# Performance work log

Hardware: AMD Instinct MI355X
Metric: run time of the kernel (lower is better)

## Reference

```python
import jax, jax.numpy as jnp
import numpy as np

INPUT_DIM, HIDDEN_DIM, N_CLASSES = 512, 256, 2
TOP_RATIO, MIN_PATCHES, K_INST = 0.7, 128, 8
B, N = 4, 16384


def setup_inputs() -> dict:
    key = jax.random.key(0)
    ks = jax.random.split(key, 10)
    D, H, C = INPUT_DIM, HIDDEN_DIM, N_CLASSES
    s = lambda fan: 1.0 / np.sqrt(fan)
    return {
        "features": jax.random.normal(ks[0], (B, N, D), dtype=jnp.float32),
        # attention_net: Linear(D->H) (dropout is identity in eval)
        "Wa": jax.random.uniform(ks[1], (D, H), minval=-s(D), maxval=s(D), dtype=jnp.float32),
        "ba": jax.random.uniform(ks[2], (H,), minval=-s(D), maxval=s(D), dtype=jnp.float32),
        # per-class attention branches: Linear(H->1), stacked over classes
        "Wbr": jax.random.uniform(ks[3], (C, H), minval=-s(H), maxval=s(H), dtype=jnp.float32),
        "bbr": jax.random.uniform(ks[4], (C,), minval=-s(H), maxval=s(H), dtype=jnp.float32),
        # per-class instance classifiers: Linear(D->H) -> ReLU -> Linear(H->2)
        "W1": jax.random.uniform(ks[5], (C, D, H), minval=-s(D), maxval=s(D), dtype=jnp.float32),
        "b1": jax.random.uniform(ks[6], (C, H), minval=-s(D), maxval=s(D), dtype=jnp.float32),
        "W2": jax.random.uniform(ks[7], (C, H, 2), minval=-s(H), maxval=s(H), dtype=jnp.float32),
        "b2": jax.random.uniform(ks[8], (C, 2), minval=-s(H), maxval=s(H), dtype=jnp.float32),
    }


def reference(features, Wa, ba, Wbr, bbr, W1, b1, W2, b2):
    Bb, Nn, D = features.shape
    C = Wbr.shape[0]

    # ---- compute_attention ----
    h = jax.nn.relu(features @ Wa + ba)                       # (B,N,H)
    a_logits = jnp.einsum('bnh,ch->bcn', h, Wbr) + bbr[None, :, None]
    attn_all = jax.nn.softmax(a_logits, axis=-1)              # (B,C,N)
    combined = attn_all.mean(axis=1)                          # (B,N)

    # ---- per-sample top-k selection (k static under jit) ----
    k = min(max(int(Nn * TOP_RATIO), MIN_PATCHES), Nn)
    _, sel_idx = jax.lax.top_k(combined, k)                   # (B,k)
    sel_idx = jnp.sort(sel_idx, axis=-1)
    selected = jnp.take_along_axis(features, sel_idx[..., None], axis=1)  # (B,k,D)

    # ---- instance clustering loss (vectorized over B x C) ----
    kk = min(K_INST, Nn // 2)
    _, top_idx = jax.lax.top_k(attn_all, kk)                  # (B,C,kk)
    _, bot_idx = jax.lax.top_k(-attn_all, kk)                 # largest=False
    both_idx = jnp.concatenate([top_idx, bot_idx], axis=-1)   # (B,C,2kk)
    inst = features[jnp.arange(Bb)[:, None, None], both_idx]  # (B,C,2kk,D)
    h1 = jax.nn.relu(jnp.einsum('bckd,cdh->bckh', inst, W1) + b1[None, :, None, :])
    logits = jnp.einsum('bckh,cho->bcko', h1, W2) + b2[None, :, None, :]  # (B,C,2kk,2)
    labels = jnp.concatenate([jnp.ones(kk, jnp.int32), jnp.zeros(kk, jnp.int32)])
    logp = jax.nn.log_softmax(logits, axis=-1)
    ce = -jnp.take_along_axis(
        logp, jnp.broadcast_to(labels[None, None, :, None], (Bb, C, 2 * kk, 1)), axis=-1
    )[..., 0]                                                 # (B,C,2kk)
    cl_loss = ce.mean(axis=-1).sum() / (Bb * C)

    return selected, combined, sel_idx, cl_loss
```

## Files before the change

### kernel.cpp

```cpp
#include <hip/hip_runtime.h>

#define NB 4
#define NP 16384
#define DD 512
#define HH 256
#define CC 2
#define KSEL 11468
#define TOTP (NB*NP)
#define BCAP 4096

#define OFF_COMB (NB*KSEL*DD)
#define OFF_IDX  (OFF_COMB + NB*NP)
#define OFF_LOSS (OFF_IDX + NB*KSEL)

#define WS_ALOGIT 0
#define WS_ATTN   (NB*CC*NP)
#define WS_SELIDX (2*NB*CC*NP)
#define WS_MZ     (WS_SELIDX + NB*KSEL)
#define WS_BCNT   (WS_MZ + 16)
#define WS_BLIST  (WS_BCNT + 4)
#define WS_TOP16  (WS_BLIST + NB*BCAP)
#define WS_CE     (WS_TOP16 + 128)

typedef __attribute__((ext_vector_type(8))) short short8x;
typedef __attribute__((ext_vector_type(4))) float f32x4;

__device__ __forceinline__ unsigned short f2bf(float x){
  unsigned u = __float_as_uint(x);
  unsigned r = (u + 0x7FFFu + ((u >> 16) & 1u)) >> 16;
  return (unsigned short)r;
}

__global__ __launch_bounds__(256) void waconv_kernel(
    const float* __restrict__ Wa, unsigned short* __restrict__ WaT)
{
  __shared__ float tile[32][33];
  const int tx = threadIdx.x, ty = threadIdx.y;
  const int k0 = blockIdx.x * 32, n0 = blockIdx.y * 32;
  #pragma unroll
  for (int i=0;i<4;++i)
    tile[ty+8*i][tx] = Wa[(size_t)(k0+ty+8*i)*HH + n0 + tx];
  __syncthreads();
  #pragma unroll
  for (int i=0;i<4;++i)
    WaT[(size_t)(n0+ty+8*i)*DD + k0 + tx] = f2bf(tile[tx][ty+8*i]);
}

__global__ __launch_bounds__(512) void gemm_mfma_kernel(
    const float* __restrict__ feat, const unsigned short* __restrict__ WaT,
    const float* __restrict__ ba, const float* __restrict__ Wbr,
    const float* __restrict__ bbr, float* __restrict__ aL)
{
  __shared__ __attribute__((aligned(16))) unsigned char smem[65536];
  __shared__ float sBA[HH], sW0[HH], sW1[HH];
  unsigned char* sA = smem;
  unsigned char* sB = smem + 16384;

  const int tid  = threadIdx.x;
  const int lane = tid & 63;
  const int wid  = tid >> 6;
  const int wm = wid >> 2, wn = wid & 3;
  const int fr = lane & 15, fq = lane >> 4;
  const int p0 = blockIdx.x * 128;
  const float bb0 = bbr[0], bb1 = bbr[1];

  if (tid < HH){ sBA[tid] = ba[tid]; sW0[tid] = Wbr[tid]; sW1[tid] = Wbr[HH+tid]; }

  f32x4 acc[4][4];
  #pragma unroll
  for (int i=0;i<4;++i)
    #pragma unroll
    for (int j=0;j<4;++j)
      acc[i][j] = (f32x4){0.f,0.f,0.f,0.f};

  const int am = tid >> 2, akq = (tid & 3) * 16;
  const int bn = tid >> 1, bhf = tid & 1;

  for (int k0 = 0; k0 < DD; k0 += 64){
    __syncthreads();
    {
      const float4* src = reinterpret_cast<const float4*>(
          feat + (size_t)(p0 + am)*DD + k0 + akq);
      float4 v0 = src[0], v1 = src[1], v2 = src[2], v3 = src[3];
      unsigned short u[16];
      u[0]=f2bf(v0.x); u[1]=f2bf(v0.y); u[2]=f2bf(v0.z); u[3]=f2bf(v0.w);
      u[4]=f2bf(v1.x); u[5]=f2bf(v1.y); u[6]=f2bf(v1.z); u[7]=f2bf(v1.w);
      u[8]=f2bf(v2.x); u[9]=f2bf(v2.y); u[10]=f2bf(v2.z); u[11]=f2bf(v2.w);
      u[12]=f2bf(v3.x); u[13]=f2bf(v3.y); u[14]=f2bf(v3.z); u[15]=f2bf(v3.w);
      uint4 w0, w1;
      w0.x = (unsigned)u[0] | ((unsigned)u[1]<<16);
      w0.y = (unsigned)u[2] | ((unsigned)u[3]<<16);
      w0.z = (unsigned)u[4] | ((unsigned)u[5]<<16);
      w0.w = (unsigned)u[6] | ((unsigned)u[7]<<16);
      w1.x = (unsigned)u[8] | ((unsigned)u[9]<<16);
      w1.y = (unsigned)u[10] | ((unsigned)u[11]<<16);
      w1.z = (unsigned)u[12] | ((unsigned)u[13]<<16);
      w1.w = (unsigned)u[14] | ((unsigned)u[15]<<16);
      const int swz = (am & 7) << 4;
      *reinterpret_cast<uint4*>(sA + (((am*128) + akq*2) ^ swz)) = w0;
      *reinterpret_cast<uint4*>(sA + (((am*128) + akq*2 + 16) ^ swz)) = w1;
    }
    {
      const uint4* src = reinterpret_cast<const uint4*>(
          WaT + (size_t)bn*DD + k0 + bhf*32);
      uint4 q0 = src[0], q1 = src[1], q2 = src[2], q3 = src[3];
      const int swz = (bn & 7) << 4;
      const int base = bn*128 + bhf*64;
      *reinterpret_cast<uint4*>(sB + ((base     ) ^ swz)) = q0;
      *reinterpret_cast<uint4*>(sB + ((base + 16) ^ swz)) = q1;
      *reinterpret_cast<uint4*>(sB + ((base + 32) ^ swz)) = q2;
      *reinterpret_cast<uint4*>(sB + ((base + 48) ^ swz)) = q3;
    }
    __syncthreads();
    #pragma unroll
    for (int kf = 0; kf < 2; ++kf){
      short8x af[4], bf[4];
      #pragma unroll
      for (int mf = 0; mf < 4; ++mf){
        int m_loc = wm*64 + mf*16 + fr;
        int off = ((m_loc*128 + kf*64 + fq*16) ^ ((m_loc & 7) << 4));
        af[mf] = *reinterpret_cast<const short8x*>(sA + off);
      }
      #pragma unroll
      for (int nf = 0; nf < 4; ++nf){
        int n_loc = wn*64 + nf*16 + fr;
        int off = ((n_loc*128 + kf*64 + fq*16) ^ ((n_loc & 7) << 4));
        bf[nf] = *reinterpret_cast<const short8x*>(sB + off);
      }
      #pragma unroll
      for (int mf = 0; mf < 4; ++mf)
        #pragma unroll
        for (int nf = 0; nf < 4; ++nf)
          acc[mf][nf] = __builtin_amdgcn_mfma_f32_16x16x32_bf16(
              af[mf], bf[nf], acc[mf][nf], 0, 0, 0);
    }
  }
  __syncthreads();

  float* hS = reinterpret_cast<float*>(smem);
  #pragma unroll
  for (int mh = 0; mh < 2; ++mh){
    if (wm == mh){
      #pragma unroll
      for (int mf = 0; mf < 4; ++mf)
        #pragma unroll
        for (int nf = 0; nf < 4; ++nf)
          #pragma unroll
          for (int r = 0; r < 4; ++r){
            int row = mf*16 + fq*4 + r;
            int col = wn*64 + nf*16 + fr;
            hS[row*256 + col] = acc[mf][nf][r];
          }
    }
    __syncthreads();
    {
      const int row = tid >> 3, cg = tid & 7;
      float s0 = 0.f, s1 = 0.f;
      #pragma unroll
      for (int j = 0; j < 8; ++j){
        int col = cg*4 + j*32;
        float4 hv = *reinterpret_cast<const float4*>(&hS[row*256 + col]);
        float xs[4] = {hv.x, hv.y, hv.z, hv.w};
        #pragma unroll
        for (int u = 0; u < 4; ++u){
          int ccol = col + u;
          float x = fmaxf(xs[u] + sBA[ccol], 0.f);
          s0 += x * sW0[ccol];
          s1 += x * sW1[ccol];
        }
      }
      s0 += __shfl_xor(s0,1); s1 += __shfl_xor(s1,1);
      s0 += __shfl_xor(s0,2); s1 += __shfl_xor(s1,2);
      s0 += __shfl_xor(s0,4); s1 += __shfl_xor(s1,4);
      if (cg == 0){
        int p = p0 + mh*64 + row;
        int b = p >> 14, nl = p & (NP-1);
        aL[((size_t)b*CC + 0)*NP + nl] = s0 + bb0;
        aL[((size_t)b*CC + 1)*NP + nl] = s1 + bb1;
      }
    }
    __syncthreads();
  }
}

__global__ __launch_bounds__(1024) void smstat_kernel(
    const float* __restrict__ aL, float* __restrict__ mz)
{
  __shared__ float  s_redf[16];
  __shared__ double s_redd[16];
  __shared__ float  s_max;
  const int tid = threadIdx.x;
  const int lane = tid & 63, wid = tid >> 6;
  const int r = blockIdx.x;
  const float* a = aL + (size_t)r*NP;
  float m = -1e30f;
  for (int n=tid; n<NP; n+=1024) m = fmaxf(m, a[n]);
  #pragma unroll
  for (int off=1; off<64; off<<=1) m = fmaxf(m, __shfl_xor(m, off));
  if (lane==0) s_redf[wid]=m;
  __syncthreads();
  if (tid==0){ float mm=s_redf[0]; for(int w=1;w<16;++w) mm=fmaxf(mm,s_redf[w]); s_max=mm; }
  __syncthreads();
  m = s_max;
  double ls = 0.0;
  for (int n=tid;n<NP;n+=1024) ls += (double)expf(a[n]-m);
  #pragma unroll
  for (int off=1; off<64; off<<=1) ls += __shfl_xor(ls, off);
  if (lane==0) s_redd[wid]=ls;
  __syncthreads();
  if (tid==0){
    double t=0; for(int w=0;w<16;++w) t+=s_redd[w];
    mz[r*2+0]=m; mz[r*2+1]=(float)(1.0/t);
  }
}

#define SKW 1028
__global__ __launch_bounds__(1024) void selTF_kernel(
    const float* __restrict__ aL, const float* __restrict__ mz,
    float* __restrict__ attn, float* __restrict__ comb,
    int* __restrict__ bcnt, int* __restrict__ blist)
{
  __shared__ unsigned s_bits[16*SKW];
  __shared__ unsigned s_red[16];
  __shared__ unsigned s_bcast;
  __shared__ int s_cnt;
  const int tid = threadIdx.x;
  const int b = blockIdx.x;
  const int lane = tid & 63, wid = tid >> 6;
  const float m0 = mz[b*4+0], iz0 = mz[b*4+1], m1 = mz[b*4+2], iz1 = mz[b*4+3];
  const float* a0 = aL + ((size_t)b*CC + 0)*NP;
  const float* a1 = aL + ((size_t)b*CC + 1)*NP;
  float* o0 = attn + ((size_t)b*CC + 0)*NP;
  float* o1 = attn + ((size_t)b*CC + 1)*NP;
  float* oc = comb + (size_t)b*NP;
  for (int j=0;j<16;++j){
    int n = tid + j*1024;
    float e0 = expf(a0[n]-m0)*iz0;
    float e1 = expf(a1[n]-m1)*iz1;
    o0[n]=e0; o1[n]=e1;
    float cv = 0.5f*(e0+e1);
    oc[n]=cv;
    s_bits[(n & 15)*SKW + (n >> 4)] = __float_as_uint(cv);
  }
  if (tid==0) s_cnt = 0;
  __syncthreads();
  unsigned cur = 0;
  for (int bit=31; bit>=12; --bit){
    unsigned trial = cur | (1u<<bit);
    int c = 0;
    #pragma unroll
    for (int j=0;j<16;++j) c += (s_bits[j*SKW + tid] >= trial) ? 1 : 0;
    #pragma unroll
    for (int off=1; off<64; off<<=1) c += __shfl_xor(c, off);
    if (lane==0) s_red[wid] = (unsigned)c;
    __syncthreads();
    if (tid==0){ unsigned t=0; for(int w=0;w<16;++w) t+=s_red[w]; s_bcast=t; }
    __syncthreads();
    if (s_bcast >= KSEL) cur = trial;
    __syncthreads();
  }
  const float Tv = __uint_as_float(cur);
  const float lo = Tv*0.989f, hi = Tv*1.0115f;
  #pragma unroll
  for (int e=0;e<16;++e){
    float v = __uint_as_float(s_bits[e*SKW + tid]);
    if (v >= lo && v <= hi){
      int s = atomicAdd(&s_cnt, 1);
      if (s < BCAP) blist[b*BCAP + s] = tid*16 + e;
    }
  }
  __syncthreads();
  if (tid==0) bcnt[b] = (s_cnt < BCAP) ? s_cnt : BCAP;
}

__global__ __launch_bounds__(256) void recomp_kernel(
    const float* __restrict__ feat, const float* __restrict__ Wa,
    const float* __restrict__ ba, const float* __restrict__ Wbr,
    const float* __restrict__ bbr, const float* __restrict__ mz,
    const int* __restrict__ bcnt, const int* __restrict__ blist,
    float* __restrict__ comb)
{
  __shared__ float fS[DD];
  __shared__ float r0[4], r1[4];
  const int tid = threadIdx.x;
  const int b = blockIdx.x >> 12;
  const int s = blockIdx.x & (BCAP-1);
  if (s >= bcnt[b]) return;
  const int lane = tid & 63, wid = tid >> 6;
  const float m0 = mz[b*4+0], iz0 = mz[b*4+1], m1 = mz[b*4+2], iz1 = mz[b*4+3];
  const int n = blist[b*BCAP + s];
  if (tid < 128){
    float4 v = *reinterpret_cast<const float4*>(feat + ((size_t)b*NP + n)*DD + tid*4);
    *reinterpret_cast<float4*>(&fS[tid*4]) = v;
  }
  __syncthreads();
  float a0=0.f,a1=0.f,a2=0.f,a3=0.f;
  #pragma unroll 4
  for (int d=0; d<DD; d+=4){
    a0 += fS[d+0]*Wa[(size_t)(d+0)*HH + tid];
    a1 += fS[d+1]*Wa[(size_t)(d+1)*HH + tid];
    a2 += fS[d+2]*Wa[(size_t)(d+2)*HH + tid];
    a3 += fS[d+3]*Wa[(size_t)(d+3)*HH + tid];
  }
  float h = fmaxf((a0+a1)+(a2+a3) + ba[tid], 0.f);
  float p0 = h*Wbr[tid], p1 = h*Wbr[HH+tid];
  #pragma unroll
  for (int off=1; off<64; off<<=1){ p0+=__shfl_xor(p0,off); p1+=__shfl_xor(p1,off); }
  if (lane==0){ r0[wid]=p0; r1[wid]=p1; }
  __syncthreads();
  if (tid==0){
    float l0 = (r0[0]+r0[1])+(r0[2]+r0[3]) + bbr[0];
    float l1 = (r1[0]+r1[1])+(r1[2]+r1[3]) + bbr[1];
    comb[(size_t)b*NP + n] = 0.5f*(expf(l0-m0)*iz0 + expf(l1-m1)*iz1);
  }
}

__global__ __launch_bounds__(1024) void select_kernel(
    const float* __restrict__ comb, float* __restrict__ outIdxF,
    int* __restrict__ selIdx)
{
  __shared__ unsigned s_bits[16*SKW];
  __shared__ unsigned s_red[16];
  __shared__ unsigned s_scan[1024];
  __shared__ unsigned s_bcast;
  const int tid = threadIdx.x;
  const int b = blockIdx.x;
  const int lane = tid & 63, wid = tid >> 6;
  const float* row = comb + (size_t)b*NP;
  for (int j=0;j<16;++j){
    int n = tid + j*1024;
    s_bits[(n & 15)*SKW + (n >> 4)] = __float_as_uint(row[n]);
  }
  __syncthreads();
  unsigned cur = 0;
  for (int bit=31; bit>=0; --bit){
    unsigned trial = cur | (1u<<bit);
    int c = 0;
    #pragma unroll
    for (int j=0;j<16;++j) c += (s_bits[j*SKW + tid] >= trial) ? 1 : 0;
    #pragma unroll
    for (int off=1; off<64; off<<=1) c += __shfl_xor(c, off);
    if (lane==0) s_red[wid] = (unsigned)c;
    __syncthreads();
    if (tid==0){ unsigned t=0; for(int w=0;w<16;++w) t+=s_red[w]; s_bcast=t; }
    __syncthreads();
    if (s_bcast >= KSEL) cur = trial;
    __syncthreads();
  }
  const unsigned T = cur;
  {
    int c = 0;
    #pragma unroll
    for (int j=0;j<16;++j) c += (s_bits[j*SKW + tid] > T) ? 1 : 0;
    #pragma unroll
    for (int off=1; off<64; off<<=1) c += __shfl_xor(c, off);
    if (lane==0) s_red[wid] = (unsigned)c;
    __syncthreads();
    if (tid==0){ unsigned t=0; for(int w=0;w<16;++w) t+=s_red[w]; s_bcast=t; }
    __syncthreads();
  }
  const int extra = KSEL - (int)s_bcast;
  __syncthreads();
  int eqc=0;
  #pragma unroll
  for (int e=0;e<16;++e) eqc += (s_bits[e*SKW + tid]==T) ? 1 : 0;
  s_scan[tid]=(unsigned)eqc;
  __syncthreads();
  for (int off=1; off<1024; off<<=1){
    unsigned v = (tid>=off)? s_scan[tid-off] : 0u;
    __syncthreads();
    s_scan[tid]+=v;
    __syncthreads();
  }
  const int eqBase = (int)s_scan[tid] - eqc;
  __syncthreads();
  int eq=eqBase, sc=0;
  #pragma unroll
  for (int e=0;e<16;++e){
    unsigned v = s_bits[e*SKW + tid];
    if (v==T){ if (eq<extra) sc++; eq++; }
    else if (v>T) sc++;
  }
  s_scan[tid]=(unsigned)sc;
  __syncthreads();
  for (int off=1; off<1024; off<<=1){
    unsigned v = (tid>=off)? s_scan[tid-off] : 0u;
    __syncthreads();
    s_scan[tid]+=v;
    __syncthreads();
  }
  int pos = (int)s_scan[tid] - sc;
  eq=eqBase;
  #pragma unroll
  for (int e=0;e<16;++e){
    unsigned v = s_bits[e*SKW + tid];
    int f=0;
    if (v==T){ if (eq<extra) f=1; eq++; }
    else if (v>T) f=1;
    if (f){
      int n = tid*16 + e;
      outIdxF[(size_t)b*KSEL + pos] = (float)n;
      selIdx[(size_t)b*KSEL + pos] = n;
      pos++;
    }
  }
}

__global__ __launch_bounds__(256) void gather_kernel(
    const float* __restrict__ feat, const int* __restrict__ selIdx,
    float* __restrict__ outSel)
{
  const int tid = threadIdx.x;
  const int row = blockIdx.x*2 + (tid>>7);
  const int c4 = tid & 127;
  const int b = row / KSEL;
  const int idx = selIdx[row];
  const float4 v = *reinterpret_cast<const float4*>(feat + ((size_t)b*NP + idx)*DD + c4*4);
  *reinterpret_cast<float4*>(outSel + (size_t)row*DD + c4*4) = v;
}

__global__ __launch_bounds__(256) void top16_kernel(
    const float* __restrict__ attn, int* __restrict__ top16)
{
  __shared__ unsigned long long wkT[4][8];
  __shared__ unsigned long long wkB[4][8];
  const int tid = threadIdx.x;
  const int bid = blockIdx.x;
  const int lane = tid & 63, wid = tid >> 6;
  const float* a = attn + (size_t)bid*NP;

  unsigned long long t8[8], b8[8];
  #pragma unroll
  for (int i=0;i<8;++i){ t8[i]=0ull; b8[i]=~0ull; }

  for (int j=0;j<16;++j){
    const int n4 = tid + 256*j;
    const float4 v = *reinterpret_cast<const float4*>(a + 4*n4);
    const float xs[4] = {v.x, v.y, v.z, v.w};
    #pragma unroll
    for (int q=0;q<4;++q){
      const int n = 4*n4 + q;
      const unsigned vb = __float_as_uint(xs[q]);
      unsigned long long kt = ((unsigned long long)vb<<32) | (unsigned)(NP-1-n);
      if (kt > t8[7]){
        t8[7]=kt;
        #pragma unroll
        for (int i=7;i>0;--i){ if (t8[i]>t8[i-1]){ unsigned long long t=t8[i-1]; t8[i-1]=t8[i]; t8[i]=t; } }
      }
      unsigned long long kb = ((unsigned long long)vb<<32) | (unsigned)n;
      if (kb < b8[7]){
        b8[7]=kb;
        #pragma unroll
        for (int i=7;i>0;--i){ if (b8[i]<b8[i-1]){ unsigned long long t=b8[i-1]; b8[i-1]=b8[i]; b8[i]=t; } }
      }
    }
  }

  #pragma unroll
  for (int pick=0; pick<8; ++pick){
    unsigned long long loc = t8[0];
    #pragma unroll
    for (int i=1;i<8;++i) loc = t8[i]>loc ? t8[i] : loc;
    #pragma unroll
    for (int off=1; off<64; off<<=1){ unsigned long long o=__shfl_xor(loc,off); loc=o>loc?o:loc; }
    if (lane==0) wkT[wid][pick]=loc;
    #pragma unroll
    for (int i=0;i<8;++i) if (t8[i]==loc) t8[i]=0ull;
  }
  #pragma unroll
  for (int pick=0; pick<8; ++pick){
    unsigned long long loc = b8[0];
    #pragma unroll
    for (int i=1;i<8;++i) loc = b8[i]<loc ? b8[i] : loc;
    #pragma unroll
    for (int off=1; off<64; off<<=1){ unsigned long long o=__shfl_xor(loc,off); loc=o<loc?o:loc; }
    if (lane==0) wkB[wid][pick]=loc;
    #pragma unroll
    for (int i=0;i<8;++i) if (b8[i]==loc) b8[i]=~0ull;
  }
  __syncthreads();

  if (wid==0){
    unsigned long long k = (lane<32) ? wkT[lane>>3][lane&7] : 0ull;
    #pragma unroll
    for (int pick=0; pick<8; ++pick){
      unsigned long long loc = k;
      #pragma unroll
      for (int off=1; off<64; off<<=1){ unsigned long long o=__shfl_xor(loc,off); loc=o>loc?o:loc; }
      if (k==loc) k=0ull;
      if (lane==0) top16[bid*16+pick] = NP-1-(int)(loc & 0xFFFFFFFFull);
    }
    unsigned long long kb = (lane<32) ? wkB[lane>>3][lane&7] : ~0ull;
    #pragma unroll
    for (int pick=0; pick<8; ++pick){
      unsigned long long loc = kb;
      #pragma unroll
      for (int off=1; off<64; off<<=1){ unsigned long long o=__shfl_xor(loc,off); loc=o<loc?o:loc; }
      if (kb==loc) kb=~0ull;
      if (lane==0) top16[bid*16+8+pick] = (int)(loc & 0xFFFFFFFFull);
    }
  }
}

__global__ __launch_bounds__(256) void mlp_kernel(
    const float* __restrict__ feat, const float* __restrict__ W1,
    const float* __restrict__ b1, const float* __restrict__ W2,
    const float* __restrict__ b2, const int* __restrict__ top16,
    float* __restrict__ cews)
{
  __shared__ float fS[DD];
  __shared__ float r0[4], r1[4];
  const int tid = threadIdx.x;
  const int bid = blockIdx.x;
  const int r = bid & 15, c = (bid >> 4) & 1, b = bid >> 5;
  const int lane = tid & 63, wid = tid >> 6;
  const int gi = top16[(b*2+c)*16 + r];
  if (tid < 128){
    float4 v = *reinterpret_cast<const float4*>(feat + ((size_t)b*NP + gi)*DD + tid*4);
    *reinterpret_cast<float4*>(&fS[tid*4]) = v;
  }
  __syncthreads();
  const float* w1c = W1 + (size_t)c*DD*HH;
  float a0=0.f,a1=0.f,a2=0.f,a3=0.f;
  #pragma unroll 4
  for (int d=0; d<DD; d+=4){
    a0 += fS[d+0]*w1c[(size_t)(d+0)*HH + tid];
    a1 += fS[d+1]*w1c[(size_t)(d+1)*HH + tid];
    a2 += fS[d+2]*w1c[(size_t)(d+2)*HH + tid];
    a3 += fS[d+3]*w1c[(size_t)(d+3)*HH + tid];
  }
  float h = fmaxf((a0+a1)+(a2+a3) + b1[c*HH+tid], 0.f);
  float p0 = h*W2[(size_t)(c*HH+tid)*2 + 0];
  float p1 = h*W2[(size_t)(c*HH+tid)*2 + 1];
  #pragma unroll
  for (int off=1; off<64; off<<=1){ p0+=__shfl_xor(p0,off); p1+=__shfl_xor(p1,off); }
  if (lane==0){ r0[wid]=p0; r1[wid]=p1; }
  __syncthreads();
  if (tid==0){
    float l0 = (r0[0]+r0[1])+(r0[2]+r0[3]) + b2[c*2+0];
    float l1 = (r1[0]+r1[1])+(r1[2]+r1[3]) + b2[c*2+1];
    float mm = fmaxf(l0,l1);
    float lse = mm + logf(expf(l0-mm)+expf(l1-mm));
    float chosen = (r<8) ? l1 : l0;
    cews[bid] = lse - chosen;
  }
}

__global__ void loss_kernel(const float* __restrict__ cews, float* __restrict__ out_loss){
  if (threadIdx.x==0 && blockIdx.x==0){
    float s=0.f;
    for (int i=0;i<128;++i) s += cews[i];
    out_loss[0] = s / 128.0f;
  }
}

extern "C" void kernel_launch(void* const* d_in, const int* in_sizes, int n_in,
                              void* d_out, int out_size, void* d_ws, size_t ws_size,
                              hipStream_t stream) {
  const float* feat = (const float*)d_in[0];
  const float* Wa   = (const float*)d_in[1];
  const float* ba   = (const float*)d_in[2];
  const float* Wbr  = (const float*)d_in[3];
  const float* bbr  = (const float*)d_in[4];
  const float* W1   = (const float*)d_in[5];
  const float* b1   = (const float*)d_in[6];
  const float* W2   = (const float*)d_in[7];
  const float* b2   = (const float*)d_in[8];
  float* out = (float*)d_out;
  float* ws  = (float*)d_ws;

  float* a_logits = ws + WS_ALOGIT;
  float* attn     = ws + WS_ATTN;
  int*   selIdx   = (int*)(ws + WS_SELIDX);
  float* mz       = ws + WS_MZ;
  int*   bcnt     = (int*)(ws + WS_BCNT);
  int*   blist    = (int*)(ws + WS_BLIST);
  int*   top16    = (int*)(ws + WS_TOP16);
  float* cews     = ws + WS_CE;

  unsigned short* WaT = (unsigned short*)d_out;

  hipLaunchKernelGGL(waconv_kernel, dim3(DD/32, HH/32), dim3(32,8), 0, stream,
                     Wa, WaT);
  hipLaunchKernelGGL(gemm_mfma_kernel, dim3(TOTP/128), dim3(512), 0, stream,
                     feat, WaT, ba, Wbr, bbr, a_logits);
  hipLaunchKernelGGL(smstat_kernel, dim3(NB*CC), dim3(1024), 0, stream,
                     a_logits, mz);
  hipLaunchKernelGGL(selTF_kernel, dim3(NB), dim3(1024), 0, stream,
                     a_logits, mz, attn, out + OFF_COMB, bcnt, blist);
  hipLaunchKernelGGL(recomp_kernel, dim3(NB*BCAP), dim3(256), 0, stream,
                     feat, Wa, ba, Wbr, bbr, mz, bcnt, blist, out + OFF_COMB);
  hipLaunchKernelGGL(select_kernel, dim3(NB), dim3(1024), 0, stream,
                     out + OFF_COMB, out + OFF_IDX, selIdx);
  hipLaunchKernelGGL(gather_kernel, dim3(NB*KSEL/2), dim3(256), 0, stream,
                     feat, selIdx, out);
  hipLaunchKernelGGL(top16_kernel, dim3(NB*CC), dim3(256), 0, stream,
                     attn, top16);
  hipLaunchKernelGGL(mlp_kernel, dim3(NB*CC*16), dim3(256), 0, stream,
                     feat, W1, b1, W2, b2, top16, cews);
  hipLaunchKernelGGL(loss_kernel, dim3(1), dim3(64), 0, stream,
                     cews, out + OFF_LOSS);
}
```

Before: 283.7 us.

## Keep top-k radix values in registers and cut block barriers per bit

The threshold-selection and index-selection kernels now keep each thread's 16 contiguous values in registers, loaded with float4, instead of staging them in a padded shared-memory array. The per-bit radix count uses a double-buffered reduction slot, so each bit needs one barrier instead of three. The 1024-entry shared-memory prefix scans are replaced by wave shuffle scans plus a per-wave sum. This removes shared-memory traffic and most synchronisation in the serial bit loops, at the cost of more register pressure and a redundant 16-way sum in every thread.

```diff
diff --git a/kernel.cpp b/kernel.cpp
--- a/kernel.cpp
+++ b/kernel.cpp
@@ -214,15 +214,12 @@
   }
 }
 
-#define SKW 1028
 __global__ __launch_bounds__(1024) void selTF_kernel(
     const float* __restrict__ aL, const float* __restrict__ mz,
     float* __restrict__ attn, float* __restrict__ comb,
     int* __restrict__ bcnt, int* __restrict__ blist)
 {
-  __shared__ unsigned s_bits[16*SKW];
-  __shared__ unsigned s_red[16];
-  __shared__ unsigned s_bcast;
+  __shared__ unsigned s_red[2][16];
   __shared__ int s_cnt;
   const int tid = threadIdx.x;
   const int b = blockIdx.x;
@@ -233,40 +230,52 @@
   float* o0 = attn + ((size_t)b*CC + 0)*NP;
   float* o1 = attn + ((size_t)b*CC + 1)*NP;
   float* oc = comb + (size_t)b*NP;
-  for (int j=0;j<16;++j){
-    int n = tid + j*1024;
-    float e0 = expf(a0[n]-m0)*iz0;
-    float e1 = expf(a1[n]-m1)*iz1;
-    o0[n]=e0; o1[n]=e1;
-    float cv = 0.5f*(e0+e1);
-    oc[n]=cv;
-    s_bits[(n & 15)*SKW + (n >> 4)] = __float_as_uint(cv);
+  const int n0 = tid*16;
+
+  unsigned v[16];
+  #pragma unroll
+  for (int g=0; g<4; ++g){
+    float4 qa = *reinterpret_cast<const float4*>(a0 + n0 + g*4);
+    float4 qb = *reinterpret_cast<const float4*>(a1 + n0 + g*4);
+    float4 E0, E1, CV;
+    E0.x = expf(qa.x-m0)*iz0; E1.x = expf(qb.x-m1)*iz1; CV.x = 0.5f*(E0.x+E1.x);
+    E0.y = expf(qa.y-m0)*iz0; E1.y = expf(qb.y-m1)*iz1; CV.y = 0.5f*(E0.y+E1.y);
+    E0.z = expf(qa.z-m0)*iz0; E1.z = expf(qb.z-m1)*iz1; CV.z = 0.5f*(E0.z+E1.z);
+    E0.w = expf(qa.w-m0)*iz0; E1.w = expf(qb.w-m1)*iz1; CV.w = 0.5f*(E0.w+E1.w);
+    *reinterpret_cast<float4*>(o0 + n0 + g*4) = E0;
+    *reinterpret_cast<float4*>(o1 + n0 + g*4) = E1;
+    *reinterpret_cast<float4*>(oc + n0 + g*4) = CV;
+    v[g*4+0]=__float_as_uint(CV.x);
+    v[g*4+1]=__float_as_uint(CV.y);
+    v[g*4+2]=__float_as_uint(CV.z);
+    v[g*4+3]=__float_as_uint(CV.w);
   }
   if (tid==0) s_cnt = 0;
-  __syncthreads();
+
   unsigned cur = 0;
+  #pragma unroll 1
   for (int bit=31; bit>=12; --bit){
     unsigned trial = cur | (1u<<bit);
     int c = 0;
     #pragma unroll
-    for (int j=0;j<16;++j) c += (s_bits[j*SKW + tid] >= trial) ? 1 : 0;
+    for (int i=0;i<16;++i) c += (v[i] >= trial) ? 1 : 0;
     #pragma unroll
     for (int off=1; off<64; off<<=1) c += __shfl_xor(c, off);
-    if (lane==0) s_red[wid] = (unsigned)c;
+    if (lane==0) s_red[bit&1][wid] = (unsigned)c;
     __syncthreads();
-    if (tid==0){ unsigned t=0; for(int w=0;w<16;++w) t+=s_red[w]; s_bcast=t; }
-    __syncthreads();
-    if (s_bcast >= KSEL) cur = trial;
-    __syncthreads();
+    unsigned tot=0;
+    #pragma unroll
+    for (int w=0;w<16;++w) tot += s_red[bit&1][w];
+    if (tot >= KSEL) cur = trial;
   }
   const float Tv = __uint_as_float(cur);
   const float lo = Tv*0.989f, hi = Tv*1.0115f;
   #pragma unroll
-  for (int e=0;e<16;++e){
-    float v = __uint_as_float(s_bits[e*SKW + tid]);
-    if (v >= lo && v <= hi){
+  for (int i=0;i<16;++i){
+    float x = __uint_as_float(v[i]);
+    if (x >= lo && x <= hi){
       int s = atomicAdd(&s_cnt, 1);
-      if (s < BCAP) blist[b*BCAP + s] = tid*16 + e;
+      if (s < BCAP) blist[b*BCAP + s] = n0 + i;
     }
   }
   __syncthreads();
@@ -319,86 +328,100 @@
     const float* __restrict__ comb, float* __restrict__ outIdxF,
     int* __restrict__ selIdx)
 {
-  __shared__ unsigned s_bits[16*SKW];
-  __shared__ unsigned s_red[16];
-  __shared__ unsigned s_scan[1024];
-  __shared__ unsigned s_bcast;
+  __shared__ unsigned s_red[2][16];
+  __shared__ unsigned s_wsum[16];
   const int tid = threadIdx.x;
   const int b = blockIdx.x;
   const int lane = tid & 63, wid = tid >> 6;
   const float* row = comb + (size_t)b*NP;
-  for (int j=0;j<16;++j){
-    int n = tid + j*1024;
-    s_bits[(n & 15)*SKW + (n >> 4)] = __float_as_uint(row[n]);
-  }
-  __syncthreads();
+
+  unsigned v[16];
+  {
+    const float4* rp = reinterpret_cast<const float4*>(row + tid*16);
+    #pragma unroll
+    for (int g=0; g<4; ++g){
+      float4 q = rp[g];
+      v[g*4+0]=__float_as_uint(q.x);
+      v[g*4+1]=__float_as_uint(q.y);
+      v[g*4+2]=__float_as_uint(q.z);
+      v[g*4+3]=__float_as_uint(q.w);
+    }
+  }
   unsigned cur = 0;
+  #pragma unroll 1
   for (int bit=31; bit>=0; --bit){
     unsigned trial = cur | (1u<<bit);
     int c = 0;
     #pragma unroll
-    for (int j=0;j<16;++j) c += (s_bits[j*SKW + tid] >= trial) ? 1 : 0;
+    for (int i=0;i<16;++i) c += (v[i] >= trial) ? 1 : 0;
     #pragma unroll
     for (int off=1; off<64; off<<=1) c += __shfl_xor(c, off);
-    if (lane==0) s_red[wid] = (unsigned)c;
+    if (lane==0) s_red[bit&1][wid] = (unsigned)c;
     __syncthreads();
-    if (tid==0){ unsigned t=0; for(int w=0;w<16;++w) t+=s_red[w]; s_bcast=t; }
-    __syncthreads();
-    if (s_bcast >= KSEL) cur = trial;
-    __syncthreads();
+    unsigned tot=0;
+    #pragma unroll
+    for (int w=0;w<16;++w) tot += s_red[bit&1][w];
+    if (tot >= KSEL) cur = trial;
   }
   const unsigned T = cur;
   {
     int c = 0;
     #pragma unroll
-    for (int j=0;j<16;++j) c += (s_bits[j*SKW + tid] > T) ? 1 : 0;
+    for (int i=0;i<16;++i) c += (v[i] > T) ? 1 : 0;
     #pragma unroll
     for (int off=1; off<64; off<<=1) c += __shfl_xor(c, off);
-    if (lane==0) s_red[wid] = (unsigned)c;
-    __syncthreads();
-    if (tid==0){ unsigned t=0; for(int w=0;w<16;++w) t+=s_red[w]; s_bcast=t; }
-    __syncthreads();
-  }
-  const int extra = KSEL - (int)s_bcast;
-  __syncthreads();
+    if (lane==0) s_red[1][wid] = (unsigned)c;
+  }
+  __syncthreads();
+  unsigned gtot=0;
+  #pragma unroll
+  for (int w=0;w<16;++w) gtot += s_red[1][w];
+  const int extra = KSEL - (int)gtot;
+
   int eqc=0;
   #pragma unroll
-  for (int e=0;e<16;++e) eqc += (s_bits[e*SKW + tid]==T) ? 1 : 0;
-  s_scan[tid]=(unsigned)eqc;
-  __syncthreads();
-  for (int off=1; off<1024; off<<=1){
-    unsigned v = (tid>=off)? s_scan[tid-off] : 0u;
-    __syncthreads();
-    s_scan[tid]+=v;
-    __syncthreads();
-  }
-  const int eqBase = (int)s_scan[tid] - eqc;
-  __syncthreads();
+  for (int i=0;i<16;++i) eqc += (v[i]==T) ? 1 : 0;
+  unsigned inc = (unsigned)eqc;
+  #pragma unroll
+  for (int off=1; off<64; off<<=1){
+    unsigned o = __shfl_up(inc, off);
+    if (lane >= off) inc += o;
+  }
+  if (lane==63) s_wsum[wid] = inc;
+  __syncthreads();
+  unsigned wbase = 0;
+  for (int w=0; w<wid; ++w) wbase += s_wsum[w];
+  const int eqBase = (int)(wbase + inc) - eqc;
+
   int eq=eqBase, sc=0;
   #pragma unroll
-  for (int e=0;e<16;++e){
-    unsigned v = s_bits[e*SKW + tid];
-    if (v==T){ if (eq<extra) sc++; eq++; }
-    else if (v>T) sc++;
-  }
-  s_scan[tid]=(unsigned)sc;
-  __syncthreads();
-  for (int off=1; off<1024; off<<=1){
-    unsigned v = (tid>=off)? s_scan[tid-off] : 0u;
-    __syncthreads();
-    s_scan[tid]+=v;
-    __syncthreads();
-  }
-  int pos = (int)s_scan[tid] - sc;
+  for (int i=0;i<16;++i){
+    unsigned x = v[i];
+    if (x==T){ if (eq<extra) sc++; eq++; }
+    else if (x>T) sc++;
+  }
+  unsigned inc2 = (unsigned)sc;
+  #pragma unroll
+  for (int off=1; off<64; off<<=1){
+    unsigned o = __shfl_up(inc2, off);
+    if (lane >= off) inc2 += o;
+  }
+  __syncthreads();
+  if (lane==63) s_wsum[wid] = inc2;
+  __syncthreads();
+  unsigned wbase2 = 0;
+  for (int w=0; w<wid; ++w) wbase2 += s_wsum[w];
+  int pos = (int)(wbase2 + inc2) - sc;
+
   eq=eqBase;
   #pragma unroll
-  for (int e=0;e<16;++e){
-    unsigned v = s_bits[e*SKW + tid];
+  for (int i=0;i<16;++i){
+    unsigned x = v[i];
     int f=0;
-    if (v==T){ if (eq<extra) f=1; eq++; }
-    else if (v>T) f=1;
+    if (x==T){ if (eq<extra) f=1; eq++; }
+    else if (x>T) f=1;
     if (f){
-      int n = tid*16 + e;
+      int n = tid*16 + i;
       outIdxF[(size_t)b*KSEL + pos] = (float)n;
       selIdx[(size_t)b*KSEL + pos] = n;
       pos++;
```

New measurement: 275.3 us. -3.0%, faster.
